# Kernel optimization log

Hardware: AMD Instinct MI355X
Metric: run time of the kernel (lower is better)

Reference implementation:

```python
import jax, jax.numpy as jnp
import numpy as np

B, C, H, W = 4, 256, 56, 56
K = 7
STRIDE = 1
DIL = 1
GROUPS = 16          # channels // group_channels(16)
GC = C // GROUPS     # 16 channels per group
PAD = (K + (K - 1) * (DIL - 1) - 1) // 2  # = 3
BN_EPS = 1e-5


def setup_inputs() -> dict:
    key = jax.random.key(0)
    ks = jax.random.split(key, 3)
    x = jax.random.normal(ks[0], (B, C, H, W), dtype=jnp.float32)
    # conv1: 1x1, C -> C//4, no bias (followed by BN)
    w1 = jax.random.normal(ks[1], (C // 4, C), dtype=jnp.float32) * (1.0 / np.sqrt(C))
    bn_gamma = jnp.ones((C // 4,), jnp.float32)
    bn_beta = jnp.zeros((C // 4,), jnp.float32)
    bn_mean = jnp.zeros((C // 4,), jnp.float32)
    bn_var = jnp.ones((C // 4,), jnp.float32)
    # conv2: 1x1, C//4 -> K*K*groups, with bias
    w2 = jax.random.normal(ks[2], (K * K * GROUPS, C // 4), dtype=jnp.float32) * (1.0 / np.sqrt(C // 4))
    b2 = jnp.zeros((K * K * GROUPS,), jnp.float32)
    return {"x": x, "w1": w1, "bn_gamma": bn_gamma, "bn_beta": bn_beta,
            "bn_mean": bn_mean, "bn_var": bn_var, "w2": w2, "b2": b2}


def _gen_weight(x, w1, bn_gamma, bn_beta, bn_mean, bn_var, w2, b2):
    # conv1 (1x1) + BN (inference stats) + ReLU
    h = jnp.einsum('oc,bchw->bohw', w1, x)
    scale = bn_gamma / jnp.sqrt(bn_var + BN_EPS)
    h = h * scale[None, :, None, None] + (bn_beta - bn_mean * scale)[None, :, None, None]
    h = jax.nn.relu(h)
    # conv2 (1x1) -> [B, K*K*groups, H, W]
    w = jnp.einsum('oc,bchw->bohw', w2, h) + b2[None, :, None, None]
    return w.reshape(B, GROUPS, K, K, H, W)


def _involution(x, weight):
    # x: [B,C,H,W], weight: [B,G,K,K,Ho,Wo]; stride=1 so Ho=H, Wo=W
    xp = jnp.pad(x, ((0, 0), (0, 0), (PAD, PAD), (PAD, PAD)))
    # gather K*K shifted views -> [B, C, K*K, H, W]
    patches = jnp.stack(
        [xp[:, :, i * DIL:i * DIL + H, j * DIL:j * DIL + W]
         for i in range(K) for j in range(K)], axis=2)
    patches = patches.reshape(B, GROUPS, GC, K * K, H, W)
    wflat = weight.reshape(B, GROUPS, K * K, H, W)
    out = jnp.einsum('bgckhw,bgkhw->bgchw', patches, wflat)
    return out.reshape(B, C, H, W)


def reference(x, w1, bn_gamma, bn_beta, bn_mean, bn_var, w2, b2):
    weight = _gen_weight(x, w1, bn_gamma, bn_beta, bn_mean, bn_var, w2, b2)
    return _involution(x, weight)
```

## Files before the change

kernel.cpp:

```cpp
#include <hip/hip_runtime.h>

typedef __attribute__((ext_vector_type(8))) short short8;
typedef __attribute__((ext_vector_type(4))) float f32x4;
typedef __attribute__((ext_vector_type(4))) unsigned int u32x4;
typedef unsigned short ushort_t;

#define BB 4
#define HW 3136
#define NX (4*256*3136)

#define K1_XB0 32768
#define K1_XB1 36864
#define K1_BIAS 40960
#define K1_SCV 41216
#define K1_TOT 41472

#define K2_B2S 28672
#define K2_TOT 28928

__device__ __forceinline__ unsigned int f2bf(float f) {
    unsigned int u = __float_as_uint(f);
    return (u + 0x7FFFu + ((u >> 16) & 1u)) >> 16;
}

__device__ __forceinline__ u32x4 pack8(f32x4 lo, f32x4 hi) {
    u32x4 r;
    r[0] = f2bf(lo[0]) | (f2bf(lo[1]) << 16);
    r[1] = f2bf(lo[2]) | (f2bf(lo[3]) << 16);
    r[2] = f2bf(hi[0]) | (f2bf(hi[1]) << 16);
    r[3] = f2bf(hi[2]) | (f2bf(hi[3]) << 16);
    return r;
}

__global__ __launch_bounds__(256) void k1_mfma(
        const float* __restrict__ x, const float* __restrict__ w1,
        const float* __restrict__ gamma, const float* __restrict__ beta,
        const float* __restrict__ mean, const float* __restrict__ var,
        ushort_t* __restrict__ h_g) {
    __shared__ __align__(16) char lds[K1_TOT];
    int blk = blockIdx.x;
    int tile = blk % 56, b = blk / 56;
    int px0 = tile * 56;
    int tid = threadIdx.x;
    int lane = tid & 63, w = tid >> 6;

    float gs = 0.f, bs = 0.f, ms = 0.f, vs = 0.f;
    if (tid < 64) { gs = gamma[tid]; bs = beta[tid]; ms = mean[tid]; vs = var[tid]; }

    int spx = tid & 63, scg = tid >> 6;
    int gpx = min(px0 + spx, HW - 1);
    const float* xbase = x + (size_t)b * 256 * HW + gpx;
    float xr[8][8];
#pragma unroll
    for (int s = 0; s < 8; s++)
#pragma unroll
        for (int u = 0; u < 8; u++)
            xr[s][u] = xbase[(size_t)(s * 32 + scg * 8 + u) * HW];

    if (tid < 64) {
        float sc = gs * rsqrtf(vs + 1e-5f);
        ((float*)(lds + K1_SCV))[tid] = sc;
        ((float*)(lds + K1_BIAS))[tid] = bs - ms * sc;
    }
    __syncthreads();

#pragma unroll
    for (int ii = 0; ii < 8; ii++) {
        int i = tid + ii * 256;
        int row = i >> 5, col8 = i & 31;
        const float* src = w1 + row * 256 + col8 * 8;
        f32x4 a = *(const f32x4*)src;
        f32x4 c = *(const f32x4*)(src + 4);
        float sc = ((const float*)(lds + K1_SCV))[row];
        unsigned int pk[4];
        pk[0] = f2bf(a[0] * sc) | (f2bf(a[1] * sc) << 16);
        pk[1] = f2bf(a[2] * sc) | (f2bf(a[3] * sc) << 16);
        pk[2] = f2bf(c[0] * sc) | (f2bf(c[1] * sc) << 16);
        pk[3] = f2bf(c[2] * sc) | (f2bf(c[3] * sc) << 16);
        u32x4 v = {pk[0], pk[1], pk[2], pk[3]};
        *(u32x4*)(lds + (row << 9) + ((col8 << 4) ^ ((row & 7) << 4))) = v;
    }

    int sdst_off = spx * 64 + ((scg << 4) ^ ((spx & 3) << 4));
    {
        unsigned int pk[4];
#pragma unroll
        for (int j = 0; j < 4; j++)
            pk[j] = f2bf(xr[0][2 * j]) | (f2bf(xr[0][2 * j + 1]) << 16);
        u32x4 v = {pk[0], pk[1], pk[2], pk[3]};
        *(u32x4*)(lds + K1_XB0 + sdst_off) = v;
    }

    f32x4 acc[4];
#pragma unroll
    for (int n = 0; n < 4; n++) acc[n] = (f32x4){0.f, 0.f, 0.f, 0.f};
    int arow = w * 16 + (lane & 15);
    int a_off = arow * 64 + (((lane >> 4) << 4) ^ ((arow & 3) << 4));

#pragma unroll
    for (int ks = 0; ks < 8; ks++) {
        __syncthreads();
        if (ks < 7) {
            unsigned int pk[4];
#pragma unroll
            for (int j = 0; j < 4; j++)
                pk[j] = f2bf(xr[ks + 1][2 * j]) | (f2bf(xr[ks + 1][2 * j + 1]) << 16);
            u32x4 v = {pk[0], pk[1], pk[2], pk[3]};
            *(u32x4*)(lds + (((ks + 1) & 1) ? K1_XB1 : K1_XB0) + sdst_off) = v;
        }
        short8 a = *(const short8*)(lds + ((ks & 1) ? K1_XB1 : K1_XB0) + a_off);
#pragma unroll
        for (int n = 0; n < 4; n++) {
            int brow = n * 16 + (lane & 15);
            short8 bb = *(const short8*)(lds + (brow << 9) +
                          ((ks * 64 + ((lane >> 4) << 4)) ^ ((brow & 7) << 4)));
            acc[n] = __builtin_amdgcn_mfma_f32_16x16x32_bf16(a, bb, acc[n], 0, 0, 0);
        }
    }

#pragma unroll
    for (int n = 0; n < 4; n++) {
        int o = n * 16 + (lane & 15);
        float bo = ((const float*)(lds + K1_BIAS))[o];
#pragma unroll
        for (int r = 0; r < 4; r++) {
            int pxl = w * 16 + ((lane >> 4) << 2) + r;
            if (pxl < 56) {
                float v = fmaxf(acc[n][r] + bo, 0.f);
                h_g[((size_t)b * HW + px0 + pxl) * 64 + o] = (ushort_t)f2bf(v);
            }
        }
    }
}

__global__ __launch_bounds__(256, 5) void k2_fused(
        const float* __restrict__ x, const ushort_t* __restrict__ h_g,
        const float* __restrict__ w2, const float* __restrict__ b2,
        float* __restrict__ out) {
    __shared__ __align__(16) char lds[K2_TOT];
    int wid0 = blockIdx.x;
    int xcd = wid0 & 7, pos = wid0 >> 3;
    int work = xcd * 112 + pos;
    int b = work / 224;
    int rem = work - b * 224;
    int half = rem / 112, r2 = rem - half * 112;
    int tloc = r2 >> 4, g = r2 & 15;
    int tile = half * 7 + tloc;
    int tid = threadIdx.x;
    int lane = tid & 63, wd = tid >> 6;

    int arow = wd * 16 + (lane & 15);
    int wrow = min(g * 49 + arow, 783);
    const float* wsrc = w2 + (size_t)wrow * 64 + ((lane >> 4) << 3);
    f32x4 a0lo = *(const f32x4*)(wsrc);
    f32x4 a0hi = *(const f32x4*)(wsrc + 4);
    f32x4 a1lo = *(const f32x4*)(wsrc + 32);
    f32x4 a1hi = *(const f32x4*)(wsrc + 36);

    const char* hg = (const char*)h_g + ((size_t)b * HW + tile * 224) * 128;
    for (int i = tid; i < 1792; i += 256) {
        int row = i >> 3, cb = (i & 7) << 4;
        u32x4 v = *(const u32x4*)(hg + row * 128 + cb);
        *(u32x4*)(lds + row * 128 + (cb ^ ((row & 7) << 4))) = v;
    }
    if (tid < 49) ((float*)(lds + K2_B2S))[tid] = b2[g * 49 + tid];

    u32x4 ap[2];
    ap[0] = pack8(a0lo, a0hi);
    ap[1] = pack8(a1lo, a1hi);
    __syncthreads();

    f32x4 acc[14];
#pragma unroll
    for (int n = 0; n < 14; n++) acc[n] = (f32x4){0.f, 0.f, 0.f, 0.f};
#pragma unroll
    for (int ks = 0; ks < 2; ks++) {
        int kc = ks * 64 + ((lane >> 4) << 4);
        short8 a = __builtin_bit_cast(short8, ap[ks]);
#pragma unroll
        for (int n = 0; n < 14; n++) {
            int brow = n * 16 + (lane & 15);
            short8 bb = *(const short8*)(lds + brow * 128 + (kc ^ ((brow & 7) << 4)));
            acc[n] = __builtin_amdgcn_mfma_f32_16x16x32_bf16(a, bb, acc[n], 0, 0, 0);
        }
    }
    __syncthreads();

    {
        const float* b2s = (const float*)(lds + K2_B2S);
        ushort_t* wl = (ushort_t*)lds;
#pragma unroll
        for (int n = 0; n < 14; n++) {
#pragma unroll
            for (int rr = 0; rr < 4; rr++) {
                int tap = wd * 16 + ((lane >> 4) << 2) + rr;
                if (tap < 49) {
                    int px = n * 16 + (lane & 15);
                    wl[tap * 232 + px] = (ushort_t)f2bf(acc[n][rr] + b2s[tap]);
                }
            }
        }
    }
    __syncthreads();

    int cpk = tid >> 5;
    int pg = tid & 31;
    int py = pg >> 3, xi = pg & 7;
    if (xi < 7) {
        int x0 = xi * 8;
        int c0 = g * 16 + cpk * 2;
        int rowb = tile * 4 + py;
        float accd[2][8];
#pragma unroll
        for (int cc = 0; cc < 2; cc++)
#pragma unroll
            for (int pi = 0; pi < 8; pi++) accd[cc][pi] = 0.f;

        for (int ky = 0; ky < 7; ky++) {
            int rr = rowb + ky - 3;
            if (rr < 0 || rr >= 56) continue;
            float w[2][16];
#pragma unroll
            for (int cc = 0; cc < 2; cc++) {
                int base = (b * 256 + c0 + cc) * HW + rr * 56 + x0 - 4;
#pragma unroll
                for (int k4 = 0; k4 < 4; k4++) {
                    int o = base + k4 * 4;
                    o = min(max(o, 0), NX - 4);
                    *(f32x4*)&w[cc][k4 * 4] = *(const f32x4*)(x + o);
                }
            }
            if (x0 == 0) {
#pragma unroll
                for (int cc = 0; cc < 2; cc++) { w[cc][1] = w[cc][2] = w[cc][3] = 0.f; }
            }
            if (x0 == 48) {
#pragma unroll
                for (int cc = 0; cc < 2; cc++) { w[cc][12] = w[cc][13] = w[cc][14] = 0.f; }
            }
#pragma unroll
            for (int kx = 0; kx < 7; kx++) {
                u32x4 wv = *(const u32x4*)(lds + ((ky * 7 + kx) * 232 + py * 56 + x0) * 2);
                float wf[8];
#pragma unroll
                for (int j = 0; j < 4; j++) {
                    wf[2 * j]     = __uint_as_float(wv[j] << 16);
                    wf[2 * j + 1] = __uint_as_float(wv[j] & 0xFFFF0000u);
                }
#pragma unroll
                for (int cc = 0; cc < 2; cc++)
#pragma unroll
                    for (int pi = 0; pi < 8; pi++)
                        accd[cc][pi] = fmaf(wf[pi], w[cc][pi + kx + 1], accd[cc][pi]);
            }
        }
#pragma unroll
        for (int cc = 0; cc < 2; cc++) {
            float* op = out + (size_t)(b * 256 + c0 + cc) * HW + tile * 224 + py * 56 + x0;
            *(f32x4*)op = (f32x4){accd[cc][0], accd[cc][1], accd[cc][2], accd[cc][3]};
            *(f32x4*)(op + 4) = (f32x4){accd[cc][4], accd[cc][5], accd[cc][6], accd[cc][7]};
        }
    }
}

extern "C" void kernel_launch(void* const* d_in, const int* in_sizes, int n_in,
                              void* d_out, int out_size, void* d_ws, size_t ws_size,
                              hipStream_t stream) {
    const float* x     = (const float*)d_in[0];
    const float* w1    = (const float*)d_in[1];
    const float* gamma = (const float*)d_in[2];
    const float* beta  = (const float*)d_in[3];
    const float* mean  = (const float*)d_in[4];
    const float* var   = (const float*)d_in[5];
    const float* w2    = (const float*)d_in[6];
    const float* b2    = (const float*)d_in[7];
    float* out = (float*)d_out;

    ushort_t* h_g = (ushort_t*)d_ws;

    k1_mfma<<<224, 256, 0, stream>>>(x, w1, gamma, beta, mean, var, h_g);
    k2_fused<<<896, 256, 0, stream>>>(x, h_g, w2, b2, out);
}
```

Before: 32.77 us.

## Rewrite conv1 kernel without LDS using direct-register MFMA over smaller pixel tiles

The first kernel now launches 896 blocks of 14 pixels each instead of 224 blocks of 56. Each wave owns 16 output channels and feeds MFMA operands straight from global loads, with no LDS staging, swizzling or barriers. The BN scale is folded into w1 per lane. This is meant to raise parallelism and remove the LDS and sync overhead, at the cost of redundant w1 loads and conversions across blocks and only 14 of 16 MFMA rows being useful. The occupancy hint on k2 also changes from 5 to 4.

```diff
diff --git a/kernel.cpp b/kernel.cpp
--- a/kernel.cpp
+++ b/kernel.cpp
@@ -8,12 +8,6 @@
 #define BB 4
 #define HW 3136
 #define NX (4*256*3136)
-
-#define K1_XB0 32768
-#define K1_XB1 36864
-#define K1_BIAS 40960
-#define K1_SCV 41216
-#define K1_TOT 41472
 
 #define K2_B2S 28672
 #define K2_TOT 28928
@@ -37,103 +31,55 @@
         const float* __restrict__ gamma, const float* __restrict__ beta,
         const float* __restrict__ mean, const float* __restrict__ var,
         ushort_t* __restrict__ h_g) {
-    __shared__ __align__(16) char lds[K1_TOT];
     int blk = blockIdx.x;
-    int tile = blk % 56, b = blk / 56;
-    int px0 = tile * 56;
+    int b = blk / 224, q = blk % 224;
+    int px0 = q * 14;
     int tid = threadIdx.x;
-    int lane = tid & 63, w = tid >> 6;
-
-    float gs = 0.f, bs = 0.f, ms = 0.f, vs = 0.f;
-    if (tid < 64) { gs = gamma[tid]; bs = beta[tid]; ms = mean[tid]; vs = var[tid]; }
-
-    int spx = tid & 63, scg = tid >> 6;
-    int gpx = min(px0 + spx, HW - 1);
-    const float* xbase = x + (size_t)b * 256 * HW + gpx;
-    float xr[8][8];
-#pragma unroll
-    for (int s = 0; s < 8; s++)
-#pragma unroll
-        for (int u = 0; u < 8; u++)
-            xr[s][u] = xbase[(size_t)(s * 32 + scg * 8 + u) * HW];
-
-    if (tid < 64) {
-        float sc = gs * rsqrtf(vs + 1e-5f);
-        ((float*)(lds + K1_SCV))[tid] = sc;
-        ((float*)(lds + K1_BIAS))[tid] = bs - ms * sc;
-    }
-    __syncthreads();
-
-#pragma unroll
-    for (int ii = 0; ii < 8; ii++) {
-        int i = tid + ii * 256;
-        int row = i >> 5, col8 = i & 31;
-        const float* src = w1 + row * 256 + col8 * 8;
-        f32x4 a = *(const f32x4*)src;
-        f32x4 c = *(const f32x4*)(src + 4);
-        float sc = ((const float*)(lds + K1_SCV))[row];
-        unsigned int pk[4];
-        pk[0] = f2bf(a[0] * sc) | (f2bf(a[1] * sc) << 16);
-        pk[1] = f2bf(a[2] * sc) | (f2bf(a[3] * sc) << 16);
-        pk[2] = f2bf(c[0] * sc) | (f2bf(c[1] * sc) << 16);
-        pk[3] = f2bf(c[2] * sc) | (f2bf(c[3] * sc) << 16);
-        u32x4 v = {pk[0], pk[1], pk[2], pk[3]};
-        *(u32x4*)(lds + (row << 9) + ((col8 << 4) ^ ((row & 7) << 4))) = v;
-    }
-
-    int sdst_off = spx * 64 + ((scg << 4) ^ ((spx & 3) << 4));
-    {
-        unsigned int pk[4];
+    int lane = tid & 63, wd = tid >> 6;
+
+    int o = wd * 16 + (lane & 15);
+    float sc = gamma[o] * rsqrtf(var[o] + 1e-5f);
+    float bo = beta[o] - mean[o] * sc;
+
+    int pxa = min(px0 + (lane & 15), HW - 1);
+    const float* xb = x + (size_t)b * 256 * HW + pxa;
+    const float* wrow = w1 + (size_t)o * 256;
+    int kb = (lane >> 4) << 3;
+
+    f32x4 acc = {0.f, 0.f, 0.f, 0.f};
+#pragma unroll 2
+    for (int ks = 0; ks < 8; ks++) {
+        int kc = ks * 32 + kb;
+        f32x4 blo = *(const f32x4*)(wrow + kc);
+        f32x4 bhi = *(const f32x4*)(wrow + kc + 4);
+        float xa[8];
+#pragma unroll
+        for (int u = 0; u < 8; u++) xa[u] = xb[(size_t)(kc + u) * HW];
+
+        u32x4 av;
 #pragma unroll
         for (int j = 0; j < 4; j++)
-            pk[j] = f2bf(xr[0][2 * j]) | (f2bf(xr[0][2 * j + 1]) << 16);
-        u32x4 v = {pk[0], pk[1], pk[2], pk[3]};
-        *(u32x4*)(lds + K1_XB0 + sdst_off) = v;
-    }
-
-    f32x4 acc[4];
-#pragma unroll
-    for (int n = 0; n < 4; n++) acc[n] = (f32x4){0.f, 0.f, 0.f, 0.f};
-    int arow = w * 16 + (lane & 15);
-    int a_off = arow * 64 + (((lane >> 4) << 4) ^ ((arow & 3) << 4));
-
-#pragma unroll
-    for (int ks = 0; ks < 8; ks++) {
-        __syncthreads();
-        if (ks < 7) {
-            unsigned int pk[4];
-#pragma unroll
-            for (int j = 0; j < 4; j++)
-                pk[j] = f2bf(xr[ks + 1][2 * j]) | (f2bf(xr[ks + 1][2 * j + 1]) << 16);
-            u32x4 v = {pk[0], pk[1], pk[2], pk[3]};
-            *(u32x4*)(lds + (((ks + 1) & 1) ? K1_XB1 : K1_XB0) + sdst_off) = v;
-        }
-        short8 a = *(const short8*)(lds + ((ks & 1) ? K1_XB1 : K1_XB0) + a_off);
-#pragma unroll
-        for (int n = 0; n < 4; n++) {
-            int brow = n * 16 + (lane & 15);
-            short8 bb = *(const short8*)(lds + (brow << 9) +
-                          ((ks * 64 + ((lane >> 4) << 4)) ^ ((brow & 7) << 4)));
-            acc[n] = __builtin_amdgcn_mfma_f32_16x16x32_bf16(a, bb, acc[n], 0, 0, 0);
-        }
-    }
-
-#pragma unroll
-    for (int n = 0; n < 4; n++) {
-        int o = n * 16 + (lane & 15);
-        float bo = ((const float*)(lds + K1_BIAS))[o];
-#pragma unroll
-        for (int r = 0; r < 4; r++) {
-            int pxl = w * 16 + ((lane >> 4) << 2) + r;
-            if (pxl < 56) {
-                float v = fmaxf(acc[n][r] + bo, 0.f);
-                h_g[((size_t)b * HW + px0 + pxl) * 64 + o] = (ushort_t)f2bf(v);
-            }
-        }
-    }
-}
-
-__global__ __launch_bounds__(256, 5) void k2_fused(
+            av[j] = f2bf(xa[2 * j]) | (f2bf(xa[2 * j + 1]) << 16);
+        f32x4 bls = {blo[0] * sc, blo[1] * sc, blo[2] * sc, blo[3] * sc};
+        f32x4 bhs = {bhi[0] * sc, bhi[1] * sc, bhi[2] * sc, bhi[3] * sc};
+        u32x4 bv = pack8(bls, bhs);
+
+        acc = __builtin_amdgcn_mfma_f32_16x16x32_bf16(
+                __builtin_bit_cast(short8, av), __builtin_bit_cast(short8, bv),
+                acc, 0, 0, 0);
+    }
+
+#pragma unroll
+    for (int r = 0; r < 4; r++) {
+        int pxr = ((lane >> 4) << 2) + r;
+        if (pxr < 14) {
+            float v = fmaxf(acc[r] + bo, 0.f);
+            h_g[((size_t)b * HW + px0 + pxr) * 64 + o] = (ushort_t)f2bf(v);
+        }
+    }
+}
+
+__global__ __launch_bounds__(256, 4) void k2_fused(
         const float* __restrict__ x, const ushort_t* __restrict__ h_g,
         const float* __restrict__ w2, const float* __restrict__ b2,
         float* __restrict__ out) {
@@ -278,6 +224,6 @@
 
     ushort_t* h_g = (ushort_t*)d_ws;
 
-    k1_mfma<<<224, 256, 0, stream>>>(x, w1, gamma, beta, mean, var, h_g);
+    k1_mfma<<<896, 256, 0, stream>>>(x, w1, gamma, beta, mean, var, h_g);
     k2_fused<<<896, 256, 0, stream>>>(x, h_g, w2, b2, out);
 }
```

Result: slower. 39.29 us (+19.9%).
